# Performance work log

Measured on AMD Instinct MI355X. Metric: run time of the kernel, lower is better.

## Reference

```python
import jax, jax.numpy as jnp
import numpy as np

N_TEAMS = 100000
N_EDGES = 1600000
BATCH = 16384
DIM = 64
SLOPE = 0.01  # torch leaky_relu default


def setup_inputs() -> dict:
    key = jax.random.key(0)
    ks = jax.random.split(key, 12)
    return {
        "edge_index": jax.random.randint(ks[0], (2, N_EDGES), 0, N_TEAMS, dtype=jnp.int32),
        "edge_weight": jax.random.uniform(ks[1], (N_EDGES,), dtype=jnp.float32),
        "home": jax.random.randint(ks[2], (BATCH,), 0, N_TEAMS, dtype=jnp.int32),
        "away": jax.random.randint(ks[3], (BATCH,), 0, N_TEAMS, dtype=jnp.int32),
        "emb": jax.random.normal(ks[4], (N_TEAMS, DIM), dtype=jnp.float32),
        "W0": jax.random.normal(ks[5], (DIM, DIM), dtype=jnp.float32) * 0.1,
        "b0": jnp.zeros((DIM,), jnp.float32),
        "W1": jax.random.normal(ks[6], (DIM, DIM), dtype=jnp.float32) * 0.1,
        "b1": jnp.zeros((DIM,), jnp.float32),
        "W2": jax.random.normal(ks[7], (DIM, DIM), dtype=jnp.float32) * 0.1,
        "b2": jnp.zeros((DIM,), jnp.float32),
        "lin1_W": jax.random.normal(ks[8], (2 * DIM, 6), dtype=jnp.float32) * 0.1,
        "lin1_b": jnp.zeros((6,), jnp.float32),
        "lin3_W": jax.random.normal(ks[9], (6, 3), dtype=jnp.float32) * 0.1,
        "lin3_b": jnp.zeros((3,), jnp.float32),
    }


def gcn_conv(x, W, b, src, dst, w, n):
    """PyG GCNConv: add self-loops, symmetric edge-weight norm, gather-scale-scatter."""
    xw = x @ W  # [N, D_out]
    loop = jnp.arange(n, dtype=src.dtype)
    src2 = jnp.concatenate([src, loop])
    dst2 = jnp.concatenate([dst, loop])
    w2 = jnp.concatenate([w, jnp.ones((n,), x.dtype)])
    deg = jax.ops.segment_sum(w2, dst2, num_segments=n)
    dinv = jnp.where(deg > 0, jax.lax.rsqrt(jnp.maximum(deg, 1e-12)), 0.0)
    norm = dinv[src2] * w2 * dinv[dst2]  # [E+N]
    msgs = norm[:, None] * xw[src2]  # irregular gather, [E+N, D_out]
    return jax.ops.segment_sum(msgs, dst2, num_segments=n) + b


def reference(edge_index, edge_weight, home, away, emb, W0, b0, W1, b1, W2, b2,
              lin1_W, lin1_b, lin3_W, lin3_b):
    src, dst = edge_index[0], edge_index[1]
    n = emb.shape[0]
    x = emb  # embedding lookup of arange(n_teams) == full table
    x = jax.nn.leaky_relu(gcn_conv(x, W0, b0, src, dst, edge_weight, n), SLOPE)
    x = jax.nn.leaky_relu(gcn_conv(x, W1, b1, src, dst, edge_weight, n), SLOPE)
    x = jax.nn.leaky_relu(gcn_conv(x, W2, b2, src, dst, edge_weight, n), SLOPE)
    h = jnp.concatenate([x[home], x[away]], axis=-1)  # [B, 2*D]
    h = jax.nn.leaky_relu(h @ lin1_W + lin1_b, SLOPE)
    h = jax.nn.leaky_relu(h @ lin3_W + lin3_b, SLOPE)
    out = jax.nn.log_softmax(h, axis=0)  # original uses LogSoftmax(dim=0)
    return out.reshape(-1, 3)
```

## Files before the change

kernel.cpp:

```cpp
#include <hip/hip_runtime.h>
#include <hip/hip_fp8.h>
#include <math.h>

#define N_TEAMS 100000
#define N_EDGES 1600000
#define BATCH   16384
#define DIM     64
#define SLOPE   0.01f
#define NPAD    100352
#define BSHIFT  6
#define BROWS   64
#define NB      1563
#define SLOTS   8
#define SCAP    384

__device__ __forceinline__ float leaky(float v) { return v > 0.f ? v : SLOPE * v; }

__device__ __forceinline__ int xcc_id() {
    int x;
    asm volatile("s_getreg_b32 %0, hwreg(HW_REG_XCC_ID)" : "=s"(x));
    return x & (SLOTS - 1);
}

__device__ __forceinline__ float bf2f(unsigned short u) {
    return __uint_as_float(((unsigned)u) << 16);
}
__device__ __forceinline__ unsigned short f2bf(float f) {
    unsigned b = __float_as_uint(f);
    unsigned r = b + 0x7FFFu + ((b >> 16) & 1u);
    return (unsigned short)(r >> 16);
}
__device__ __forceinline__ float f82f(unsigned char u) {
    __hip_fp8_e4m3 v; v.__x = (__hip_fp8_storage_t)u;
    return (float)v;
}
__device__ __forceinline__ unsigned char f2f8(float f) {
    __hip_fp8_e4m3 v(f);
    return (unsigned char)v.__x;
}
__device__ __forceinline__ float pw2f(unsigned p) {
    return __uint_as_float((p & 0xFFFE0000u) >> 1);
}


__global__ void k_zerob(int* __restrict__ bcnt) {
    int i = blockIdx.x * blockDim.x + threadIdx.x;
    if (i < NB * SLOTS) bcnt[i * 16] = 0;
}

__global__ void k_part(const int* __restrict__ src, const int* __restrict__ dst,
                       const float* __restrict__ w, int* __restrict__ bcnt,
                       unsigned long long* __restrict__ pbuf, int E) {
    int e = blockIdx.x * blockDim.x + threadIdx.x;
    if (e >= E) return;
    int slot = xcc_id();
    int s = __builtin_nontemporal_load(src + e);
    int d = __builtin_nontemporal_load(dst + e);
    float wv = __builtin_nontemporal_load(w + e);
    unsigned pk = (((unsigned)f2bf(wv) & 0x7FFFu) << 17) | (unsigned)s;
    int cell = (d >> BSHIFT) * SLOTS + slot;
    int p = atomicAdd(&bcnt[cell * 16], 1);
    if (p < SCAP) pbuf[(size_t)cell * SCAP + p] = (((unsigned long long)d) << 32) | pk;
}

__global__ __launch_bounds__(256) void k_bcnt(const int* __restrict__ bcnt,
                                              const unsigned long long* __restrict__ pbuf,
                                              int* __restrict__ cnt,
                                              float* __restrict__ dinv) {
    __shared__ int h[BROWS];
    __shared__ float ws[BROWS];
    int b = blockIdx.x, tid = threadIdx.x;
    if (tid < BROWS) { h[tid] = 0; ws[tid] = 0.f; }
    __syncthreads();
    for (int slot = 0; slot < SLOTS; slot++) {
        int cell = b * SLOTS + slot;
        int n = bcnt[cell * 16];
        const unsigned long long* pb = pbuf + (size_t)cell * SCAP;
        for (int i = tid; i < n; i += 256) {
            unsigned long long rec = pb[i];
            int d = (int)(rec >> 32);
            atomicAdd(&h[d & (BROWS - 1)], 1);
            atomicAdd(&ws[d & (BROWS - 1)], pw2f((unsigned)rec));
        }
    }
    __syncthreads();
    int row = b * BROWS + tid;
    if (tid < BROWS && row < NPAD) {
        cnt[row] = h[tid];
        dinv[row] = rsqrtf(fmaxf(1.0f + ws[tid], 1e-12f));
    }
}

__global__ __launch_bounds__(256) void k_scatter(const int* __restrict__ bcnt,
                                                 const unsigned long long* __restrict__ pbuf,
                                                 const int* __restrict__ row_start,
                                                 unsigned* __restrict__ edges) {
    __shared__ int fl[BROWS];
    int b = blockIdx.x, tid = threadIdx.x;
    if (tid < BROWS) fl[tid] = 0;
    __syncthreads();
    for (int slot = 0; slot < SLOTS; slot++) {
        int cell = b * SLOTS + slot;
        int n = bcnt[cell * 16];
        const unsigned long long* pb = pbuf + (size_t)cell * SCAP;
        for (int i = tid; i < n; i += 256) {
            unsigned long long rec = pb[i];
            int d = (int)(rec >> 32);
            int p = atomicAdd(&fl[d & (BROWS - 1)], 1);
            edges[row_start[d] + p] = (unsigned)rec;
        }
    }
}


__global__ __launch_bounds__(1024) void k_scan1(const int* __restrict__ cnt,
                                                int* __restrict__ excl,
                                                int* __restrict__ partial, int n) {
    __shared__ int s[1024];
    int tid = threadIdx.x;
    int i = blockIdx.x * 1024 + tid;
    int v = (i < n) ? cnt[i] : 0;
    s[tid] = v;
    __syncthreads();
    for (int off = 1; off < 1024; off <<= 1) {
        int t = (tid >= off) ? s[tid - off] : 0;
        __syncthreads();
        s[tid] += t;
        __syncthreads();
    }
    excl[i] = s[tid] - v;
    if (tid == 1023) partial[blockIdx.x] = s[1023];
}

__global__ __launch_bounds__(128) void k_scan2(int* __restrict__ partial, int nb) {
    __shared__ int s[128];
    int tid = threadIdx.x;
    int v = (tid < nb) ? partial[tid] : 0;
    s[tid] = v;
    __syncthreads();
    for (int off = 1; off < 128; off <<= 1) {
        int t = (tid >= off) ? s[tid - off] : 0;
        __syncthreads();
        s[tid] += t;
        __syncthreads();
    }
    if (tid < nb) partial[tid] = s[tid] - v;
}

__global__ __launch_bounds__(1024) void k_scan3(int* __restrict__ row_start,
                                                const int* __restrict__ partial) {
    int i = blockIdx.x * 1024 + threadIdx.x;
    row_start[i] += partial[blockIdx.x];
}


__global__ void k_cvt(const float* __restrict__ emb, unsigned short* __restrict__ y,
                      int n4) {
    int i = blockIdx.x * blockDim.x + threadIdx.x;
    if (i >= n4) return;
    float4 v = ((const float4*)emb)[i];
    ushort4 o;
    o.x = f2bf(v.x); o.y = f2bf(v.y); o.z = f2bf(v.z); o.w = f2bf(v.w);
    ((ushort4*)y)[i] = o;
}


__global__ __launch_bounds__(256) void k_gemm(
    const unsigned short* __restrict__ y, const float* __restrict__ W,
    const float* __restrict__ dinv, unsigned char* __restrict__ t8, int n) {
    __shared__ float Ws[64 * 64];
    __shared__ float xs[16 * 64];
    int tid = threadIdx.x;
    const float4* Wv = (const float4*)W;
    float4* Wsv = (float4*)Ws;
#pragma unroll
    for (int i = 0; i < 4; i++) Wsv[tid + i * 256] = Wv[tid + i * 256];
    int row0 = blockIdx.x * 16;
    {
        int idx = tid * 4;
        int r = idx >> 6, cc = idx & 63;
        ushort4 v = *(const ushort4*)(y + (((size_t)(row0 + r)) << 6) + cc);
        xs[idx + 0] = bf2f(v.x); xs[idx + 1] = bf2f(v.y);
        xs[idx + 2] = bf2f(v.z); xs[idx + 3] = bf2f(v.w);
    }
    __syncthreads();
    int c = tid & 63, rr = tid >> 6;
    float acc[4] = {0.f, 0.f, 0.f, 0.f};
#pragma unroll
    for (int k = 0; k < 64; k++) {
        float wv = Ws[k * 64 + c];
#pragma unroll
        for (int i = 0; i < 4; i++) acc[i] = fmaf(xs[(4 * i + rr) * 64 + k], wv, acc[i]);
    }
#pragma unroll
    for (int i = 0; i < 4; i++) {
        int r = row0 + 4 * i + rr;
        t8[(((size_t)r) << 6) + c] = f2f8(dinv[r] * acc[i]);
    }
}


__global__ __launch_bounds__(256) void k_agg(
    const unsigned char* __restrict__ t8, const int* __restrict__ row_start,
    const unsigned* __restrict__ edges, const float* __restrict__ dinv,
    const float* __restrict__ b, unsigned short* __restrict__ y, int n) {
    int tid = threadIdx.x;
    int lane = tid & 63;
    int row = blockIdx.x * 4 + (tid >> 6);
    if (row >= n) return;
    float bl = b[lane];
    int beg = row_start[row];
    int c = row_start[row + 1] - beg;
    float di = dinv[row];
    float acc = f82f(t8[((unsigned)row << 6) + lane]);
    const unsigned* ep = edges + beg;
    int j = 0;
    int chunks = c >> 3;
    if (chunks > 0) {
        unsigned ev[8];
#pragma unroll
        for (int k = 0; k < 8; k++) ev[k] = __builtin_nontemporal_load(ep + k);
        for (int t = 1; t <= chunks; t++) {
            float nv[8], xv[8];
#pragma unroll
            for (int k = 0; k < 8; k++) {
                int s = (int)(ev[k] & 0x1FFFFu);
                nv[k] = pw2f(ev[k]);
                xv[k] = f82f(t8[((unsigned)s << 6) + lane]);
            }
            if (t < chunks) {
                const unsigned* np = ep + (size_t)t * 8;
#pragma unroll
                for (int k = 0; k < 8; k++) ev[k] = __builtin_nontemporal_load(np + k);
            }
#pragma unroll
            for (int k = 0; k < 8; k++) acc = fmaf(nv[k], xv[k], acc);
        }
        j = chunks * 8;
    }
    if (j + 4 <= c) {
        unsigned e0 = __builtin_nontemporal_load(ep + j + 0);
        unsigned e1 = __builtin_nontemporal_load(ep + j + 1);
        unsigned e2 = __builtin_nontemporal_load(ep + j + 2);
        unsigned e3 = __builtin_nontemporal_load(ep + j + 3);
        float x0 = f82f(t8[((e0 & 0x1FFFFu) << 6) + lane]);
        float x1 = f82f(t8[((e1 & 0x1FFFFu) << 6) + lane]);
        float x2 = f82f(t8[((e2 & 0x1FFFFu) << 6) + lane]);
        float x3 = f82f(t8[((e3 & 0x1FFFFu) << 6) + lane]);
        acc = fmaf(pw2f(e0), x0, acc);
        acc = fmaf(pw2f(e1), x1, acc);
        acc = fmaf(pw2f(e2), x2, acc);
        acc = fmaf(pw2f(e3), x3, acc);
        j += 4;
    }
    for (; j < c; j++) {
        unsigned e0 = __builtin_nontemporal_load(ep + j);
        acc = fmaf(pw2f(e0), f82f(t8[((e0 & 0x1FFFFu) << 6) + lane]), acc);
    }
    y[((unsigned)row << 6) + lane] = f2bf(leaky(fmaf(di, acc, bl)));
}


__global__ __launch_bounds__(256) void k_head(
    const unsigned short* __restrict__ xb, const int* __restrict__ home,
    const int* __restrict__ away, const float* __restrict__ W1,
    const float* __restrict__ b1, const float* __restrict__ W3,
    const float* __restrict__ b3, float* __restrict__ z2, int B) {
    __shared__ float W1s[128 * 6];
    __shared__ float b1s[6], W3s[18], b3s[3];
    int tid = threadIdx.x;
    for (int i = tid; i < 768; i += 256) W1s[i] = W1[i];
    if (tid < 6) b1s[tid] = b1[tid];
    if (tid < 18) W3s[tid] = W3[tid];
    if (tid < 3) b3s[tid] = b3[tid];
    __syncthreads();
    int i = blockIdx.x * 256 + tid;
    if (i >= B) return;
    float z1[6];
#pragma unroll
    for (int j = 0; j < 6; j++) z1[j] = b1s[j];
    const uint4* rows[2];
    rows[0] = (const uint4*)(xb + (size_t)home[i] * 64);
    rows[1] = (const uint4*)(xb + (size_t)away[i] * 64);
#pragma unroll
    for (int h = 0; h < 2; h++) {
        const uint4* r = rows[h];
        int base = h * 64;
#pragma unroll
        for (int k = 0; k < 8; k++) {
            uint4 v = r[k];
            unsigned uu[4] = {v.x, v.y, v.z, v.w};
#pragma unroll
            for (int t = 0; t < 4; t++) {
                float fx = bf2f((unsigned short)(uu[t] & 0xFFFF));
                float fy = bf2f((unsigned short)(uu[t] >> 16));
                int d = base + k * 8 + t * 2;
#pragma unroll
                for (int j = 0; j < 6; j++) {
                    z1[j] = fmaf(fx, W1s[d * 6 + j], z1[j]);
                    z1[j] = fmaf(fy, W1s[(d + 1) * 6 + j], z1[j]);
                }
            }
        }
    }
#pragma unroll
    for (int j = 0; j < 6; j++) z1[j] = leaky(z1[j]);
#pragma unroll
    for (int c = 0; c < 3; c++) {
        float s = b3s[c];
#pragma unroll
        for (int j = 0; j < 6; j++) s = fmaf(z1[j], W3s[j * 3 + c], s);
        z2[(size_t)i * 3 + c] = leaky(s);
    }
}


__global__ __launch_bounds__(1024) void k_stats(const float* __restrict__ z2,
                                                float* __restrict__ stats, int B) {
    __shared__ float red[3][1024];
    int tid = threadIdx.x;
    float m[3] = {-1e30f, -1e30f, -1e30f};
    for (int i = tid; i < B; i += 1024) {
        m[0] = fmaxf(m[0], z2[3 * i + 0]);
        m[1] = fmaxf(m[1], z2[3 * i + 1]);
        m[2] = fmaxf(m[2], z2[3 * i + 2]);
    }
    for (int c = 0; c < 3; c++) red[c][tid] = m[c];
    __syncthreads();
    for (int s = 512; s > 0; s >>= 1) {
        if (tid < s)
            for (int c = 0; c < 3; c++) red[c][tid] = fmaxf(red[c][tid], red[c][tid + s]);
        __syncthreads();
    }
    float M[3];
    for (int c = 0; c < 3; c++) M[c] = red[c][0];
    __syncthreads();
    float sum[3] = {0.f, 0.f, 0.f};
    for (int i = tid; i < B; i += 1024) {
        sum[0] += expf(z2[3 * i + 0] - M[0]);
        sum[1] += expf(z2[3 * i + 1] - M[1]);
        sum[2] += expf(z2[3 * i + 2] - M[2]);
    }
    for (int c = 0; c < 3; c++) red[c][tid] = sum[c];
    __syncthreads();
    for (int s = 512; s > 0; s >>= 1) {
        if (tid < s)
            for (int c = 0; c < 3; c++) red[c][tid] += red[c][tid + s];
        __syncthreads();
    }
    if (tid == 0)
        for (int c = 0; c < 3; c++) { stats[c] = M[c]; stats[3 + c] = logf(red[c][0]); }
}

__global__ void k_final(const float* __restrict__ z2, const float* __restrict__ stats,
                        float* __restrict__ out, int n) {
    int i = blockIdx.x * blockDim.x + threadIdx.x;
    if (i < n) {
        int c = i % 3;
        out[i] = z2[i] - stats[c] - stats[3 + c];
    }
}


extern "C" void kernel_launch(void* const* d_in, const int* in_sizes, int n_in,
                              void* d_out, int out_size, void* d_ws, size_t ws_size,
                              hipStream_t stream) {
    const int*   edge_index = (const int*)d_in[0];
    const int*   src  = edge_index;
    const int*   dst  = edge_index + N_EDGES;
    const float* ew   = (const float*)d_in[1];
    const int*   home = (const int*)d_in[2];
    const int*   away = (const int*)d_in[3];
    const float* emb  = (const float*)d_in[4];
    const float* W0 = (const float*)d_in[5];  const float* b0 = (const float*)d_in[6];
    const float* W1 = (const float*)d_in[7];  const float* b1 = (const float*)d_in[8];
    const float* W2 = (const float*)d_in[9];  const float* b2 = (const float*)d_in[10];
    const float* l1W = (const float*)d_in[11]; const float* l1b = (const float*)d_in[12];
    const float* l3W = (const float*)d_in[13]; const float* l3b = (const float*)d_in[14];

    char* p = (char*)d_ws;
    float*              dinv      = (float*)p;              p += NPAD * 4;
    int*                cnt       = (int*)p;                p += NPAD * 4;
    int*                row_start = (int*)p;                p += (NPAD + 1024) * 4;
    int*                partial   = (int*)p;                p += 128 * 4;
    int*                bcnt      = (int*)p;                p += (size_t)NB * SLOTS * 16 * 4;
    unsigned*           edges     = (unsigned*)p;           p += (size_t)N_EDGES * 4;
    unsigned char*      t8        = (unsigned char*)p;      p += (size_t)N_TEAMS * 64;
    unsigned short*     Y         = (unsigned short*)p;     p += (size_t)N_TEAMS * 64 * 2;
    unsigned long long* pbuf      = (unsigned long long*)p; p += (size_t)NB * SLOTS * SCAP * 8;
    float*              z2        = (float*)p;              p += (size_t)BATCH * 3 * 4;
    float*              stats     = (float*)p;

    const int scanBlocks = NPAD / 1024;

    k_zerob<<<(NB * SLOTS + 255) / 256, 256, 0, stream>>>(bcnt);
    k_part<<<(N_EDGES + 255) / 256, 256, 0, stream>>>(src, dst, ew, bcnt, pbuf, N_EDGES);
    k_bcnt<<<NB, 256, 0, stream>>>(bcnt, pbuf, cnt, dinv);
    k_scan1<<<scanBlocks, 1024, 0, stream>>>(cnt, row_start, partial, N_TEAMS);
    k_scan2<<<1, 128, 0, stream>>>(partial, scanBlocks);
    k_scan3<<<scanBlocks, 1024, 0, stream>>>(row_start, partial);
    k_scatter<<<NB, 256, 0, stream>>>(bcnt, pbuf, row_start, edges);
    k_cvt<<<(N_TEAMS * 16 + 255) / 256, 256, 0, stream>>>(emb, Y, N_TEAMS * 16);

    const int GBLOCKS = N_TEAMS / 16;
    const int ABLOCKS = (N_TEAMS + 3) / 4;

    k_gemm<<<GBLOCKS, 256, 0, stream>>>(Y, W0, dinv, t8, N_TEAMS);
    k_agg<<<ABLOCKS, 256, 0, stream>>>(t8, row_start, edges, dinv, b0, Y, N_TEAMS);
    k_gemm<<<GBLOCKS, 256, 0, stream>>>(Y, W1, dinv, t8, N_TEAMS);
    k_agg<<<ABLOCKS, 256, 0, stream>>>(t8, row_start, edges, dinv, b1, Y, N_TEAMS);
    k_gemm<<<GBLOCKS, 256, 0, stream>>>(Y, W2, dinv, t8, N_TEAMS);
    k_agg<<<ABLOCKS, 256, 0, stream>>>(t8, row_start, edges, dinv, b2, Y, N_TEAMS);

    k_head<<<(BATCH + 255) / 256, 256, 0, stream>>>(Y, home, away, l1W, l1b, l3W, l3b, z2, BATCH);
    k_stats<<<1, 1024, 0, stream>>>(z2, stats, BATCH);
    k_final<<<(BATCH * 3 + 255) / 256, 256, 0, stream>>>(z2, stats, (float*)d_out, BATCH * 3);
}
```

Baseline: 412.0 us.

## Pack partition records into 32 bits with 9-bit weight code; fuse embedding conversion

Edge weights are now stored as a custom 9-bit log-style code. This frees room to hold the low 6 bits of the destination row in the same 32-bit word, so the partition buffer shrinks from 64-bit to 32-bit records, cutting traffic in the partition, count and scatter passes. The first GEMM now reads the fp32 embedding directly, removing the separate bf16 conversion kernel and its round trip. The trade-off is lower weight precision (5-bit mantissa, with small weights flushed to zero) and extra decode arithmetic in the aggregation inner loop.

```diff
diff --git a/kernel.cpp b/kernel.cpp
--- a/kernel.cpp
+++ b/kernel.cpp
@@ -38,8 +38,19 @@
     __hip_fp8_e4m3 v(f);
     return (unsigned char)v.__x;
 }
-__device__ __forceinline__ float pw2f(unsigned p) {
-    return __uint_as_float((p & 0xFFFE0000u) >> 1);
+__device__ __forceinline__ unsigned enc9(float w) {
+    unsigned bits = __float_as_uint(w);
+    int exp = (int)((bits >> 23) & 0xFF) - 127;
+    int ec = -1 - exp;
+    unsigned mr = ((bits & 0x7FFFFFu) + (1u << 17)) >> 18;
+    if (mr == 32) { mr = 0; ec -= 1; }
+    if (ec < 0) { ec = 0; mr = 31; }
+    return (ec > 14) ? (15u << 5) : (((unsigned)ec << 5) | mr);
+}
+__device__ __forceinline__ float dec9(unsigned u9) {
+    unsigned ec = (u9 >> 5) & 0xF, m = u9 & 31u;
+    if (ec == 15u) return 0.f;
+    return __uint_as_float(((126u - ec) << 23) | (m << 18));
 }
 
 
@@ -50,21 +61,21 @@
 
 __global__ void k_part(const int* __restrict__ src, const int* __restrict__ dst,
                        const float* __restrict__ w, int* __restrict__ bcnt,
-                       unsigned long long* __restrict__ pbuf, int E) {
+                       unsigned* __restrict__ pbuf, int E) {
     int e = blockIdx.x * blockDim.x + threadIdx.x;
     if (e >= E) return;
     int slot = xcc_id();
     int s = __builtin_nontemporal_load(src + e);
     int d = __builtin_nontemporal_load(dst + e);
     float wv = __builtin_nontemporal_load(w + e);
-    unsigned pk = (((unsigned)f2bf(wv) & 0x7FFFu) << 17) | (unsigned)s;
+    unsigned rec = (enc9(wv) << 23) | (((unsigned)d & 63u) << 17) | (unsigned)s;
     int cell = (d >> BSHIFT) * SLOTS + slot;
     int p = atomicAdd(&bcnt[cell * 16], 1);
-    if (p < SCAP) pbuf[(size_t)cell * SCAP + p] = (((unsigned long long)d) << 32) | pk;
+    if (p < SCAP) pbuf[(size_t)cell * SCAP + p] = rec;
 }
 
 __global__ __launch_bounds__(256) void k_bcnt(const int* __restrict__ bcnt,
-                                              const unsigned long long* __restrict__ pbuf,
+                                              const unsigned* __restrict__ pbuf,
                                               int* __restrict__ cnt,
                                               float* __restrict__ dinv) {
     __shared__ int h[BROWS];
@@ -75,12 +86,12 @@
     for (int slot = 0; slot < SLOTS; slot++) {
         int cell = b * SLOTS + slot;
         int n = bcnt[cell * 16];
-        const unsigned long long* pb = pbuf + (size_t)cell * SCAP;
+        const unsigned* pb = pbuf + (size_t)cell * SCAP;
         for (int i = tid; i < n; i += 256) {
-            unsigned long long rec = pb[i];
-            int d = (int)(rec >> 32);
-            atomicAdd(&h[d & (BROWS - 1)], 1);
-            atomicAdd(&ws[d & (BROWS - 1)], pw2f((unsigned)rec));
+            unsigned rec = pb[i];
+            int d6 = (rec >> 17) & 63;
+            atomicAdd(&h[d6], 1);
+            atomicAdd(&ws[d6], dec9(rec >> 23));
         }
     }
     __syncthreads();
@@ -92,22 +103,23 @@
 }
 
 __global__ __launch_bounds__(256) void k_scatter(const int* __restrict__ bcnt,
-                                                 const unsigned long long* __restrict__ pbuf,
+                                                 const unsigned* __restrict__ pbuf,
                                                  const int* __restrict__ row_start,
                                                  unsigned* __restrict__ edges) {
     __shared__ int fl[BROWS];
     int b = blockIdx.x, tid = threadIdx.x;
     if (tid < BROWS) fl[tid] = 0;
     __syncthreads();
+    int base = b * BROWS;
     for (int slot = 0; slot < SLOTS; slot++) {
         int cell = b * SLOTS + slot;
         int n = bcnt[cell * 16];
-        const unsigned long long* pb = pbuf + (size_t)cell * SCAP;
+        const unsigned* pb = pbuf + (size_t)cell * SCAP;
         for (int i = tid; i < n; i += 256) {
-            unsigned long long rec = pb[i];
-            int d = (int)(rec >> 32);
-            int p = atomicAdd(&fl[d & (BROWS - 1)], 1);
-            edges[row_start[d] + p] = (unsigned)rec;
+            unsigned rec = pb[i];
+            int d6 = (rec >> 17) & 63;
+            int p = atomicAdd(&fl[d6], 1);
+            edges[row_start[base + d6] + p] = rec;
         }
     }
 }
@@ -154,16 +166,37 @@
 }
 
 
-__global__ void k_cvt(const float* __restrict__ emb, unsigned short* __restrict__ y,
-                      int n4) {
-    int i = blockIdx.x * blockDim.x + threadIdx.x;
-    if (i >= n4) return;
-    float4 v = ((const float4*)emb)[i];
-    ushort4 o;
-    o.x = f2bf(v.x); o.y = f2bf(v.y); o.z = f2bf(v.z); o.w = f2bf(v.w);
-    ((ushort4*)y)[i] = o;
-}
-
+__global__ __launch_bounds__(256) void k_gemm_f32(
+    const float* __restrict__ x, const float* __restrict__ W,
+    const float* __restrict__ dinv, unsigned char* __restrict__ t8, int n) {
+    __shared__ float Ws[64 * 64];
+    __shared__ float xs[16 * 64];
+    int tid = threadIdx.x;
+    const float4* Wv = (const float4*)W;
+    float4* Wsv = (float4*)Ws;
+#pragma unroll
+    for (int i = 0; i < 4; i++) Wsv[tid + i * 256] = Wv[tid + i * 256];
+    int row0 = blockIdx.x * 16;
+    {
+        float4 v = ((const float4*)(x + ((size_t)row0 << 6)))[tid];
+        float4* xo = (float4*)xs;
+        xo[tid] = v;
+    }
+    __syncthreads();
+    int c = tid & 63, rr = tid >> 6;
+    float acc[4] = {0.f, 0.f, 0.f, 0.f};
+#pragma unroll
+    for (int k = 0; k < 64; k++) {
+        float wv = Ws[k * 64 + c];
+#pragma unroll
+        for (int i = 0; i < 4; i++) acc[i] = fmaf(xs[(4 * i + rr) * 64 + k], wv, acc[i]);
+    }
+#pragma unroll
+    for (int i = 0; i < 4; i++) {
+        int r = row0 + 4 * i + rr;
+        t8[(((size_t)r) << 6) + c] = f2f8(dinv[r] * acc[i]);
+    }
+}
 
 __global__ __launch_bounds__(256) void k_gemm(
     const unsigned short* __restrict__ y, const float* __restrict__ W,
@@ -225,7 +258,7 @@
 #pragma unroll
             for (int k = 0; k < 8; k++) {
                 int s = (int)(ev[k] & 0x1FFFFu);
-                nv[k] = pw2f(ev[k]);
+                nv[k] = dec9(ev[k] >> 23);
                 xv[k] = f82f(t8[((unsigned)s << 6) + lane]);
             }
             if (t < chunks) {
@@ -247,15 +280,15 @@
         float x1 = f82f(t8[((e1 & 0x1FFFFu) << 6) + lane]);
         float x2 = f82f(t8[((e2 & 0x1FFFFu) << 6) + lane]);
         float x3 = f82f(t8[((e3 & 0x1FFFFu) << 6) + lane]);
-        acc = fmaf(pw2f(e0), x0, acc);
-        acc = fmaf(pw2f(e1), x1, acc);
-        acc = fmaf(pw2f(e2), x2, acc);
-        acc = fmaf(pw2f(e3), x3, acc);
+        acc = fmaf(dec9(e0 >> 23), x0, acc);
+        acc = fmaf(dec9(e1 >> 23), x1, acc);
+        acc = fmaf(dec9(e2 >> 23), x2, acc);
+        acc = fmaf(dec9(e3 >> 23), x3, acc);
         j += 4;
     }
     for (; j < c; j++) {
         unsigned e0 = __builtin_nontemporal_load(ep + j);
-        acc = fmaf(pw2f(e0), f82f(t8[((e0 & 0x1FFFFu) << 6) + lane]), acc);
+        acc = fmaf(dec9(e0 >> 23), f82f(t8[((e0 & 0x1FFFFu) << 6) + lane]), acc);
     }
     y[((unsigned)row << 6) + lane] = f2bf(leaky(fmaf(di, acc, bl)));
 }
@@ -379,17 +412,17 @@
     const float* l3W = (const float*)d_in[13]; const float* l3b = (const float*)d_in[14];
 
     char* p = (char*)d_ws;
-    float*              dinv      = (float*)p;              p += NPAD * 4;
-    int*                cnt       = (int*)p;                p += NPAD * 4;
-    int*                row_start = (int*)p;                p += (NPAD + 1024) * 4;
-    int*                partial   = (int*)p;                p += 128 * 4;
-    int*                bcnt      = (int*)p;                p += (size_t)NB * SLOTS * 16 * 4;
-    unsigned*           edges     = (unsigned*)p;           p += (size_t)N_EDGES * 4;
-    unsigned char*      t8        = (unsigned char*)p;      p += (size_t)N_TEAMS * 64;
-    unsigned short*     Y         = (unsigned short*)p;     p += (size_t)N_TEAMS * 64 * 2;
-    unsigned long long* pbuf      = (unsigned long long*)p; p += (size_t)NB * SLOTS * SCAP * 8;
-    float*              z2        = (float*)p;              p += (size_t)BATCH * 3 * 4;
-    float*              stats     = (float*)p;
+    float*          dinv      = (float*)p;          p += NPAD * 4;
+    int*            cnt       = (int*)p;            p += NPAD * 4;
+    int*            row_start = (int*)p;            p += (NPAD + 1024) * 4;
+    int*            partial   = (int*)p;            p += 128 * 4;
+    int*            bcnt      = (int*)p;            p += (size_t)NB * SLOTS * 16 * 4;
+    unsigned*       edges     = (unsigned*)p;       p += (size_t)N_EDGES * 4;
+    unsigned char*  t8        = (unsigned char*)p;  p += (size_t)N_TEAMS * 64;
+    unsigned short* Y         = (unsigned short*)p; p += (size_t)N_TEAMS * 64 * 2;
+    unsigned*       pbuf      = (unsigned*)p;       p += (size_t)NB * SLOTS * SCAP * 4;
+    float*          z2        = (float*)p;          p += (size_t)BATCH * 3 * 4;
+    float*          stats     = (float*)p;
 
     const int scanBlocks = NPAD / 1024;
 
@@ -400,12 +433,11 @@
     k_scan2<<<1, 128, 0, stream>>>(partial, scanBlocks);
     k_scan3<<<scanBlocks, 1024, 0, stream>>>(row_start, partial);
     k_scatter<<<NB, 256, 0, stream>>>(bcnt, pbuf, row_start, edges);
-    k_cvt<<<(N_TEAMS * 16 + 255) / 256, 256, 0, stream>>>(emb, Y, N_TEAMS * 16);
 
     const int GBLOCKS = N_TEAMS / 16;
     const int ABLOCKS = (N_TEAMS + 3) / 4;
 
-    k_gemm<<<GBLOCKS, 256, 0, stream>>>(Y, W0, dinv, t8, N_TEAMS);
+    k_gemm_f32<<<GBLOCKS, 256, 0, stream>>>(emb, W0, dinv, t8, N_TEAMS);
     k_agg<<<ABLOCKS, 256, 0, stream>>>(t8, row_start, edges, dinv, b0, Y, N_TEAMS);
     k_gemm<<<GBLOCKS, 256, 0, stream>>>(Y, W1, dinv, t8, N_TEAMS);
     k_agg<<<ABLOCKS, 256, 0, stream>>>(t8, row_start, edges, dinv, b1, Y, N_TEAMS);
```

Measured after the change: 411.0 us. Within noise of the previous version (-0.2%).
